# Kernel tuning notes

Hardware: AMD Instinct MI355X
Metric: run time of the kernel (lower is better)

Reference implementation:

```python
import math
import jax, jax.numpy as jnp
import numpy as np

LN_EPS = 1e-5


def _layernorm(x, g, b):
    m = jnp.mean(x, axis=-1, keepdims=True)
    v = jnp.var(x, axis=-1, keepdims=True)
    return (x - m) / jnp.sqrt(v + LN_EPS) * g + b


def setup_inputs() -> dict:
    key = jax.random.key(0)
    ks = jax.random.split(key, 14)
    B, C, H, W = 8, 96, 224, 224
    dim, hidden = 96, int(96 * 4.0)

    def lin(k, i, o):
        return jax.random.normal(k, (i, o), jnp.float32) * 0.02

    return {
        "x": jax.random.normal(ks[0], (B, C, H, W), jnp.float32),
        "entropy_map": jax.random.uniform(ks[1], (B, 1, H, W), jnp.float32),
        "beta": jnp.float32(1.0),
        "wq": lin(ks[2], dim, dim), "bq": jnp.zeros((dim,), jnp.float32),
        "wk": lin(ks[3], dim, dim), "bk": jnp.zeros((dim,), jnp.float32),
        "wv": lin(ks[4], dim, dim), "bv": jnp.zeros((dim,), jnp.float32),
        "wo": lin(ks[5], dim, dim), "bo": jnp.zeros((dim,), jnp.float32),
        "ln1_g": jnp.ones((dim,), jnp.float32), "ln1_b": jnp.zeros((dim,), jnp.float32),
        "ln2_g": jnp.ones((dim,), jnp.float32), "ln2_b": jnp.zeros((dim,), jnp.float32),
        "w_fc1": lin(ks[6], dim, hidden), "b_fc1": jnp.zeros((hidden,), jnp.float32),
        "w_fc2": lin(ks[7], hidden, dim), "b_fc2": jnp.zeros((dim,), jnp.float32),
    }


def reference(x, entropy_map, beta, wq, bq, wk, bk, wv, bv, wo, bo,
              ln1_g, ln1_b, ln2_g, ln2_b, w_fc1, b_fc1, w_fc2, b_fc2):
    B, C, H, W = x.shape
    ws = 7
    num_heads = 4
    hd = C // num_heads
    nHw, nWw = H // ws, W // ws
    N = ws * ws

    # (B,C,H,W) -> (B,H,W,C), norm1
    xt = jnp.transpose(x, (0, 2, 3, 1))
    xn = _layernorm(xt, ln1_g, ln1_b)

    # window partition -> (B*nW, N, C)
    xw = xn.reshape(B, nHw, ws, nWw, ws, C).transpose(0, 1, 3, 2, 4, 5).reshape(-1, N, C)
    ew = entropy_map.transpose(0, 2, 3, 1).reshape(B, nHw, ws, nWw, ws, 1)
    ew = ew.transpose(0, 1, 3, 2, 4, 5).reshape(-1, N, 1)  # (Bw, N, 1)

    Bw = xw.shape[0]
    q = (jnp.einsum('bnc,cd->bnd', xw, wq) + bq).reshape(Bw, N, num_heads, hd).transpose(0, 2, 1, 3)
    k = (jnp.einsum('bnc,cd->bnd', xw, wk) + bk).reshape(Bw, N, num_heads, hd).transpose(0, 2, 1, 3)
    v = (jnp.einsum('bnc,cd->bnd', xw, wv) + bv).reshape(Bw, N, num_heads, hd).transpose(0, 2, 1, 3)

    scores = jnp.einsum('bhqd,bhkd->bhqk', q, k) / math.sqrt(hd)
    attn = jax.nn.softmax(scores, axis=-1)

    # entropy gating: per-query factor (Bw,1,N,1), then renormalize over keys
    gating = jnp.exp(-beta * ew)[:, None, :, :]
    attn = attn * gating
    attn = attn / (jnp.sum(attn, axis=-1, keepdims=True) + 1e-9)

    out = jnp.einsum('bhqk,bhkd->bhqd', attn, v).transpose(0, 2, 1, 3).reshape(Bw, N, C)
    out = jnp.einsum('bnc,cd->bnd', out, wo) + bo

    # window merge -> (B,H,W,C)
    out = out.reshape(B, nHw, nWw, ws, ws, C).transpose(0, 1, 3, 2, 4, 5).reshape(B, H, W, C)

    x_res = xt + out  # (B,H,W,C)

    # MLP branch
    xn2 = _layernorm(x_res, ln2_g, ln2_b)
    h = jax.nn.gelu(jnp.einsum('bhwc,cd->bhwd', xn2, w_fc1) + b_fc1, approximate=False)
    mlp_out = jnp.einsum('bhwd,dc->bhwc', h, w_fc2) + b_fc2

    x_out = x_res + mlp_out
    return jnp.transpose(x_out, (0, 3, 1, 2))  # (B,C,H,W)
```

## Files before the change

### kernel.cpp

```cpp
#include <hip/hip_runtime.h>
#include <hip/hip_bf16.h>
#include <math.h>

typedef __attribute__((ext_vector_type(8))) short short8;
typedef __attribute__((ext_vector_type(4))) float f32x4;
typedef __attribute__((ext_vector_type(4))) unsigned int uint4v;

struct __align__(8) U2 { unsigned int x, y; };

#define DEVI static __device__ __forceinline__

DEVI unsigned pk1(float f){ unsigned u = __float_as_uint(f); return (u + 0x7fffu + ((u>>16)&1u)) >> 16; }
DEVI unsigned pk2(float a, float b){
  __hip_bfloat162 h = __float22bfloat162_rn(float2{a, b});
  union { __hip_bfloat162 h; unsigned u; } c; c.h = h; return c.u;
}
DEVI float bfu(unsigned hs){ return __uint_as_float((hs & 0xffffu) << 16); }

DEVI short8 lds8(const unsigned short* p){
  union { short8 v; U2 u[2]; } f;
  f.u[0] = *(const U2*)p;
  f.u[1] = *(const U2*)(p + 4);
  return f.v;
}
DEVI short8 mk8(unsigned a, unsigned b, unsigned c, unsigned d){
  union { short8 v; unsigned u[4]; } f; f.u[0]=a; f.u[1]=b; f.u[2]=c; f.u[3]=d; return f.v;
}
DEVI short8 zero8(){ return mk8(0,0,0,0); }
DEVI short8 gfrag(const unsigned short* p){ union { short8 v; uint4v u; } f; f.u = *(const uint4v*)p; return f.v; }
DEVI f32x4 MFMA(short8 a, short8 b, f32x4 c){ return __builtin_amdgcn_mfma_f32_16x16x32_bf16(a, b, c, 0, 0, 0); }
DEVI void st2(unsigned short* p, unsigned lo, unsigned hi){ U2 t; t.x=lo; t.y=hi; *(U2*)p = t; }

DEVI float fastrcp(float x){ float r; asm("v_rcp_f32 %0, %1" : "=v"(r) : "v"(x)); return r; }
DEVI float gelu_f(float v){
  float z2 = fmaf(v*v*v, -0.07135481627f, -1.5957691216f*v);
  return v * fastrcp(1.f + __expf(z2));
}

__global__ __launch_bounds__(256) void prep_kernel(
    const float* __restrict__ wq, const float* __restrict__ wk,
    const float* __restrict__ wv, const float* __restrict__ wo,
    const float* __restrict__ w1, const float* __restrict__ w2,
    unsigned short* __restrict__ wfr)
{
  int i = blockIdx.x * 256 + threadIdx.x;
  if (i >= 110592) return;
  int j = i & 7, lane = (i >> 3) & 63, fr = i >> 9;
  int ln = lane & 15, lg = lane >> 4;
  float v;
  if (fr < 18)      { int s = fr;       int mt = s/3,  kb = s%3;  v = wq[(32*kb + 8*lg + j)*96  + 16*mt + ln] * 0.20412414523193150818f; }
  else if (fr < 36) { int s = fr - 18;  int mt = s/3,  kb = s%3;  v = wk[(32*kb + 8*lg + j)*96  + 16*mt + ln]; }
  else if (fr < 54) { int s = fr - 36;  int mt = s/3,  kb = s%3;  v = wv[(32*kb + 8*lg + j)*96  + 16*mt + ln]; }
  else if (fr < 72) { int s = fr - 54;  int mt = s/3,  kb = s%3;  v = wo[(32*kb + 8*lg + j)*96  + 16*mt + ln]; }
  else if (fr < 144){ int s = fr - 72;  int mt = s/3,  kb = s%3;  v = w1[(32*kb + 8*lg + j)*384 + 16*mt + ln]; }
  else              { int s = fr - 144; int mt = s/12, kb = s%12; v = w2[(32*kb + 8*lg + j)*96  + 16*mt + ln]; }
  wfr[i] = (unsigned short)pk1(v);
}

__global__ __launch_bounds__(256, 3) void attn_kernel(
    const float* __restrict__ x, const float* __restrict__ emap,
    const float* __restrict__ beta_p,
    const float* __restrict__ bq, const float* __restrict__ bk,
    const float* __restrict__ bv, const float* __restrict__ bo,
    const float* __restrict__ g1, const float* __restrict__ b1,
    const unsigned short* __restrict__ wfr,
    unsigned short* __restrict__ xres)
{
  __shared__ __align__(16) char smem[52544];
  unsigned short* XN = (unsigned short*)(smem);
  unsigned short* QS = (unsigned short*)(smem + 12800);
  unsigned short* KS = (unsigned short*)(smem + 25600);
  unsigned short* VT = (unsigned short*)(smem + 38400);

  const int tid = threadIdx.x;
  const int lane = tid & 63;
  const int w = tid >> 6, lg = lane >> 4, ln = lane & 15;

  int bid = blockIdx.x;
  int bw  = ((bid & 7) << 10) | (bid >> 3);
  const int b  = bw >> 10;
  const int rr = bw & 1023;
  const int h0w = (rr >> 5) * 7;
  const int w0w = (rr & 31) * 7;

  const int t = 16*w + ln;

  float xv[24];
  float ewv = 0.f;
  {
    if (t < 49){
      size_t pixloc = (size_t)(h0w + t/7)*224 + w0w + t%7;
      const float* xp = x + (size_t)(b*96 + 4*lg)*50176 + pixloc;
#pragma unroll
      for (int mt = 0; mt < 6; ++mt)
#pragma unroll
        for (int r = 0; r < 4; ++r) xv[mt*4+r] = xp[(size_t)(16*mt + r)*50176];
      ewv = emap[(size_t)b*50176 + pixloc];
    } else {
#pragma unroll
      for (int i = 0; i < 24; ++i) xv[i] = 0.f;
    }
    float s = 0.f, s2 = 0.f;
#pragma unroll
    for (int i = 0; i < 24; ++i){ s += xv[i]; s2 += xv[i]*xv[i]; }
    s  += __shfl_xor(s, 16);  s  += __shfl_xor(s, 32);
    s2 += __shfl_xor(s2, 16); s2 += __shfl_xor(s2, 32);
    float m = s * (1.f/96.f);
    float var = s2 * (1.f/96.f) - m*m;
    float rstd = rsqrtf(var + 1e-5f);
    unsigned short* row = XN + t*100;
    if (t < 49){
#pragma unroll
      for (int mt = 0; mt < 6; ++mt){
        int c0 = 16*mt + 4*lg;
        st2(row + c0,
            pk2((xv[4*mt+0]-m)*rstd*g1[c0+0]+b1[c0+0], (xv[4*mt+1]-m)*rstd*g1[c0+1]+b1[c0+1]),
            pk2((xv[4*mt+2]-m)*rstd*g1[c0+2]+b1[c0+2], (xv[4*mt+3]-m)*rstd*g1[c0+3]+b1[c0+3]));
      }
    } else {
#pragma unroll
      for (int mt = 0; mt < 6; ++mt) st2(row + 16*mt + 4*lg, 0u, 0u);
    }
  }
  __syncthreads();

  {
    short8 bx0 = lds8(XN + t*100 + 0  + 8*lg);
    short8 bx1 = lds8(XN + t*100 + 32 + 8*lg);
    short8 bx2 = lds8(XN + t*100 + 64 + 8*lg);
#pragma unroll
    for (int mt = 0; mt < 6; ++mt){
      int d0 = 16*mt + 4*lg;
      f32x4 aq, ak;
#pragma unroll
      for (int r = 0; r < 4; ++r){ aq[r] = bq[d0+r]*0.20412414523193150818f; ak[r] = bk[d0+r]; }
      aq = MFMA(gfrag(wfr +        (mt*3+0)*512 + lane*8), bx0, aq);
      aq = MFMA(gfrag(wfr +        (mt*3+1)*512 + lane*8), bx1, aq);
      aq = MFMA(gfrag(wfr +        (mt*3+2)*512 + lane*8), bx2, aq);
      ak = MFMA(gfrag(wfr + 9216 + (mt*3+0)*512 + lane*8), bx0, ak);
      ak = MFMA(gfrag(wfr + 9216 + (mt*3+1)*512 + lane*8), bx1, ak);
      ak = MFMA(gfrag(wfr + 9216 + (mt*3+2)*512 + lane*8), bx2, ak);
      st2(QS + t*100 + d0, pk2(aq[0],aq[1]), pk2(aq[2],aq[3]));
      st2(KS + t*100 + d0, pk2(ak[0],ak[1]), pk2(ak[2],ak[3]));
    }
#pragma unroll
    for (int f = 0; f < 6; ++f){
      int fl = f*4 + w;
      int mt = fl / 6, nt = fl % 6;
      float bvv = bv[16*nt + ln];
      f32x4 av; av[0]=bvv; av[1]=bvv; av[2]=bvv; av[3]=bvv;
#pragma unroll
      for (int kb = 0; kb < 3; ++kb)
        av = MFMA(lds8(XN + (16*mt+ln)*100 + 32*kb + 8*lg),
                  gfrag(wfr + 18432 + (nt*3+kb)*512 + lane*8), av);
      st2(VT + (16*nt+ln)*68 + 16*mt + 4*lg, pk2(av[0],av[1]), pk2(av[2],av[3]));
    }
  }
  __syncthreads();

  const float beta = beta_p[0];
  const float gq   = __expf(-beta * ewv);
  const float gfac = gq / (gq + 1e-9f);
  const int  psrcA = ((lg & 1) << 5) + ln;
  const int  psrcB = psrcA + 16;
  const bool phi   = (lg >= 2);

  f32x4 mz;  mz[0]=0.f; mz[1]=0.f; mz[2]=0.f; mz[3]=0.f;
  f32x4 m3;
#pragma unroll
  for (int r = 0; r < 4; ++r) m3[r] = (4*lg + r >= 1) ? -50.f : 0.f;

#pragma unroll
  for (int hp = 0; hp < 2; ++hp){
    const int h0 = 2*hp, h1 = 2*hp + 1;

    short8 bqf0 = (lg < 3) ? lds8(QS + t*100 + 24*h0 + 8*lg) : zero8();
    short8 bqf1 = (lg < 3) ? lds8(QS + t*100 + 24*h1 + 8*lg) : zero8();
    f32x4 sv0[4], sv1[4];
#pragma unroll
    for (int mt = 0; mt < 4; ++mt){
      short8 af0 = (lg < 3) ? lds8(KS + (16*mt+ln)*100 + 24*h0 + 8*lg) : zero8();
      short8 af1 = (lg < 3) ? lds8(KS + (16*mt+ln)*100 + 24*h1 + 8*lg) : zero8();
      f32x4 ci = (mt == 3) ? m3 : mz;
      sv0[mt] = MFMA(af0, bqf0, ci);
      sv1[mt] = MFMA(af1, bqf1, ci);
    }

    float vv0[16], vv1[16];
    float ss0 = 0.f, ss1 = 0.f;
#pragma unroll
    for (int i = 0; i < 16; ++i){
      float e0 = __expf(sv0[i>>2][i&3]); vv0[i] = e0; ss0 += e0;
      float e1 = __expf(sv1[i>>2][i&3]); vv1[i] = e1; ss1 += e1;
    }
    ss0 += __shfl_xor(ss0, 16);  ss1 += __shfl_xor(ss1, 16);
    ss0 += __shfl_xor(ss0, 32);  ss1 += __shfl_xor(ss1, 32);
    float inv0 = gfac * fastrcp(ss0);
    float inv1 = gfac * fastrcp(ss1);

    unsigned pu0[4][2], pu1[4][2];
#pragma unroll
    for (int mt = 0; mt < 4; ++mt){
      pu0[mt][0] = pk2(vv0[4*mt+0], vv0[4*mt+1]);
      pu0[mt][1] = pk2(vv0[4*mt+2], vv0[4*mt+3]);
      pu1[mt][0] = pk2(vv1[4*mt+0], vv1[4*mt+1]);
      pu1[mt][1] = pk2(vv1[4*mt+2], vv1[4*mt+3]);
    }

    unsigned a00=__shfl(pu0[0][0],psrcA), a01=__shfl(pu0[0][1],psrcA);
    unsigned e00=__shfl(pu1[0][0],psrcA), e01=__shfl(pu1[0][1],psrcA);
    unsigned a10=__shfl(pu0[1][0],psrcA), a11=__shfl(pu0[1][1],psrcA);
    unsigned e10=__shfl(pu1[1][0],psrcA), e11=__shfl(pu1[1][1],psrcA);
    unsigned b00=__shfl(pu0[0][0],psrcB), b01=__shfl(pu0[0][1],psrcB);
    unsigned f00=__shfl(pu1[0][0],psrcB), f01=__shfl(pu1[0][1],psrcB);
    unsigned b10=__shfl(pu0[1][0],psrcB), b11=__shfl(pu0[1][1],psrcB);
    unsigned f10=__shfl(pu1[1][0],psrcB), f11=__shfl(pu1[1][1],psrcB);
    short8 pf00 = mk8(phi?a10:a00, phi?a11:a01, phi?b10:b00, phi?b11:b01);
    short8 pf10 = mk8(phi?e10:e00, phi?e11:e01, phi?f10:f00, phi?f11:f01);
    unsigned c00=__shfl(pu0[2][0],psrcA), c01=__shfl(pu0[2][1],psrcA);
    unsigned g00=__shfl(pu1[2][0],psrcA), g01=__shfl(pu1[2][1],psrcA);
    unsigned c10=__shfl(pu0[3][0],psrcA), c11=__shfl(pu0[3][1],psrcA);
    unsigned g10=__shfl(pu1[3][0],psrcA), g11=__shfl(pu1[3][1],psrcA);
    unsigned d00=__shfl(pu0[2][0],psrcB), d01=__shfl(pu0[2][1],psrcB);
    unsigned k00=__shfl(pu1[2][0],psrcB), k01=__shfl(pu1[2][1],psrcB);
    unsigned d10=__shfl(pu0[3][0],psrcB), d11=__shfl(pu0[3][1],psrcB);
    unsigned k10=__shfl(pu1[3][0],psrcB), k11=__shfl(pu1[3][1],psrcB);
    short8 pf01 = mk8(phi?c10:c00, phi?c11:c01, phi?d10:d00, phi?d11:d01);
    short8 pf11 = mk8(phi?g10:g00, phi?g11:g01, phi?k10:k00, phi?k11:k01);

#pragma unroll
    for (int mt = 0; mt < 2; ++mt){
      f32x4 pv0; pv0[0]=0.f; pv0[1]=0.f; pv0[2]=0.f; pv0[3]=0.f;
      f32x4 pv1; pv1[0]=0.f; pv1[1]=0.f; pv1[2]=0.f; pv1[3]=0.f;
      pv0 = MFMA(lds8(VT + (24*h0+16*mt+ln)*68 + 0  + 8*lg), pf00, pv0);
      pv1 = MFMA(lds8(VT + (24*h1+16*mt+ln)*68 + 0  + 8*lg), pf10, pv1);
      pv0 = MFMA(lds8(VT + (24*h0+16*mt+ln)*68 + 32 + 8*lg), pf01, pv0);
      pv1 = MFMA(lds8(VT + (24*h1+16*mt+ln)*68 + 32 + 8*lg), pf11, pv1);
      if (!(mt == 1 && lg >= 2)){
        st2(XN + t*100 + 24*h0 + 16*mt + 4*lg,
            pk2(pv0[0]*inv0, pv0[1]*inv0), pk2(pv0[2]*inv0, pv0[3]*inv0));
        st2(XN + t*100 + 24*h1 + 16*mt + 4*lg,
            pk2(pv1[0]*inv1, pv1[1]*inv1), pk2(pv1[2]*inv1, pv1[3]*inv1));
      }
    }
  }

  {
    f32x4 po[6];
#pragma unroll
    for (int mt = 0; mt < 6; ++mt){
      int c0 = 16*mt + 4*lg;
#pragma unroll
      for (int r = 0; r < 4; ++r) po[mt][r] = bo[c0+r];
    }
#pragma unroll
    for (int kb = 0; kb < 3; ++kb){
      short8 bf_ = lds8(XN + t*100 + 32*kb + 8*lg);
#pragma unroll
      for (int mt = 0; mt < 6; ++mt)
        po[mt] = MFMA(gfrag(wfr + 27648 + (mt*3+kb)*512 + lane*8), bf_, po[mt]);
    }
    if (t < 49){
      size_t pixloc = (size_t)(h0w + t/7)*224 + w0w + t%7;
      unsigned short* xo = xres + ((size_t)b*50176 + pixloc)*96;
#pragma unroll
      for (int mt = 0; mt < 6; ++mt){
        int c0 = 16*mt + 4*lg;
        st2(xo + c0,
            pk2(po[mt][0] + xv[4*mt+0], po[mt][1] + xv[4*mt+1]),
            pk2(po[mt][2] + xv[4*mt+2], po[mt][3] + xv[4*mt+3]));
      }
    }
  }
}

__global__ __launch_bounds__(256, 3) void mlp_kernel(
    const unsigned short* __restrict__ xres,
    const float* __restrict__ g2, const float* __restrict__ b2,
    const float* __restrict__ bf1, const float* __restrict__ bf2,
    const unsigned short* __restrict__ wfr,
    float* __restrict__ out)
{
  __shared__ __align__(16) unsigned short XH[4][6400];
  const int tid = threadIdx.x, lane = tid & 63, w = tid >> 6;
  const int lg = lane >> 4, ln = lane & 15;
  unsigned short* XN2 = &XH[w][0];
  unsigned short* HS  = &XH[w][3200];

  const int tile = blockIdx.x*4 + w;
  const size_t p0 = (size_t)tile * 32;
  const int bimg = (int)(p0 / 50176);
  const size_t pixin = p0 - (size_t)bimg*50176;

#pragma unroll
  for (int s = 0; s < 2; ++s){
    const unsigned* xp = (const unsigned*)(xres + (p0 + 16*s + (size_t)ln)*96 + 24*lg);
    float xv[24];
#pragma unroll
    for (int i = 0; i < 12; ++i){
      unsigned u = xp[i];
      xv[2*i] = bfu(u); xv[2*i+1] = bfu(u >> 16);
    }
    float sm = 0.f, s2 = 0.f;
#pragma unroll
    for (int i = 0; i < 24; ++i){ sm += xv[i]; s2 += xv[i]*xv[i]; }
    sm += __shfl_xor(sm, 16);  sm += __shfl_xor(sm, 32);
    s2 += __shfl_xor(s2, 16);  s2 += __shfl_xor(s2, 32);
    float m = sm * (1.f/96.f);
    float var = s2 * (1.f/96.f) - m*m;
    float rstd = rsqrtf(var + 1e-5f);
    unsigned* w32 = (unsigned*)(XN2 + (16*s + ln)*100 + 24*lg);
#pragma unroll
    for (int i = 0; i < 12; ++i){
      int c = 24*lg + 2*i;
      w32[i] = pk2((xv[2*i]   - m)*rstd*g2[c]   + b2[c],
                   (xv[2*i+1] - m)*rstd*g2[c+1] + b2[c+1]);
    }
  }

  f32x4 oaccA[6], oaccB[6];
#pragma unroll
  for (int mt = 0; mt < 6; ++mt){
    int c0 = 16*mt + 4*lg;
#pragma unroll
    for (int r = 0; r < 4; ++r){ oaccA[mt][r] = bf2[c0+r]; oaccB[mt][r] = bf2[c0+r]; }
  }

  short8 bxA0 = lds8(XN2 + ln*100 + 0  + 8*lg);
  short8 bxA1 = lds8(XN2 + ln*100 + 32 + 8*lg);
  short8 bxA2 = lds8(XN2 + ln*100 + 64 + 8*lg);
  short8 bxB0 = lds8(XN2 + (16+ln)*100 + 0  + 8*lg);
  short8 bxB1 = lds8(XN2 + (16+ln)*100 + 32 + 8*lg);
  short8 bxB2 = lds8(XN2 + (16+ln)*100 + 64 + 8*lg);

#pragma unroll
  for (int p = 0; p < 4; ++p){
#pragma unroll
    for (int mt = 0; mt < 6; ++mt){
      int hg = p*96 + 16*mt + 4*lg;
      f32x4 hA, hB;
#pragma unroll
      for (int r = 0; r < 4; ++r){ hA[r] = bf1[hg+r]; hB[r] = bf1[hg+r]; }
      short8 a0 = gfrag(wfr + 36864 + ((p*6+mt)*3+0)*512 + lane*8);
      short8 a1 = gfrag(wfr + 36864 + ((p*6+mt)*3+1)*512 + lane*8);
      short8 a2 = gfrag(wfr + 36864 + ((p*6+mt)*3+2)*512 + lane*8);
      hA = MFMA(a0, bxA0, hA); hB = MFMA(a0, bxB0, hB);
      hA = MFMA(a1, bxA1, hA); hB = MFMA(a1, bxB1, hB);
      hA = MFMA(a2, bxA2, hA); hB = MFMA(a2, bxB2, hB);
      st2(HS + ln*100 + 16*mt + 4*lg,
          pk2(gelu_f(hA[0]), gelu_f(hA[1])), pk2(gelu_f(hA[2]), gelu_f(hA[3])));
      st2(HS + (16+ln)*100 + 16*mt + 4*lg,
          pk2(gelu_f(hB[0]), gelu_f(hB[1])), pk2(gelu_f(hB[2]), gelu_f(hB[3])));
    }
#pragma unroll
    for (int kb = 0; kb < 3; ++kb){
      short8 bhA = lds8(HS + ln*100      + 32*kb + 8*lg);
      short8 bhB = lds8(HS + (16+ln)*100 + 32*kb + 8*lg);
#pragma unroll
      for (int mt = 0; mt < 6; ++mt){
        short8 af = gfrag(wfr + 73728 + (mt*12 + p*3 + kb)*512 + lane*8);
        oaccA[mt] = MFMA(af, bhA, oaccA[mt]);
        oaccB[mt] = MFMA(af, bhB, oaccB[mt]);
      }
    }
  }

  {
    const unsigned short* xrA = xres + (p0 + (size_t)ln)*96;
    const unsigned short* xrB = xrA + 16*96;
    float* obA = out + (size_t)bimg*96*50176 + pixin + ln;
    float* obB = obA + 16;
#pragma unroll
    for (int mt = 0; mt < 6; ++mt){
      int c0 = 16*mt + 4*lg;
      U2 rA = *(const U2*)(xrA + c0);
      U2 rB = *(const U2*)(xrB + c0);
      obA[(size_t)(c0+0)*50176] = oaccA[mt][0] + bfu(rA.x);
      obA[(size_t)(c0+1)*50176] = oaccA[mt][1] + bfu(rA.x >> 16);
      obA[(size_t)(c0+2)*50176] = oaccA[mt][2] + bfu(rA.y);
      obA[(size_t)(c0+3)*50176] = oaccA[mt][3] + bfu(rA.y >> 16);
      obB[(size_t)(c0+0)*50176] = oaccB[mt][0] + bfu(rB.x);
      obB[(size_t)(c0+1)*50176] = oaccB[mt][1] + bfu(rB.x >> 16);
      obB[(size_t)(c0+2)*50176] = oaccB[mt][2] + bfu(rB.y);
      obB[(size_t)(c0+3)*50176] = oaccB[mt][3] + bfu(rB.y >> 16);
    }
  }
}

extern "C" void kernel_launch(void* const* d_in, const int* in_sizes, int n_in,
                              void* d_out, int out_size, void* d_ws, size_t ws_size,
                              hipStream_t stream) {
  const float* x    = (const float*)d_in[0];
  const float* emap = (const float*)d_in[1];
  const float* beta = (const float*)d_in[2];
  const float* wq   = (const float*)d_in[3];
  const float* bq   = (const float*)d_in[4];
  const float* wk   = (const float*)d_in[5];
  const float* bk   = (const float*)d_in[6];
  const float* wv   = (const float*)d_in[7];
  const float* bv   = (const float*)d_in[8];
  const float* wo   = (const float*)d_in[9];
  const float* bo   = (const float*)d_in[10];
  const float* g1   = (const float*)d_in[11];
  const float* b1   = (const float*)d_in[12];
  const float* g2   = (const float*)d_in[13];
  const float* b2   = (const float*)d_in[14];
  const float* w1   = (const float*)d_in[15];
  const float* bf1  = (const float*)d_in[16];
  const float* w2   = (const float*)d_in[17];
  const float* bf2  = (const float*)d_in[18];

  float* out = (float*)d_out;
  unsigned short* wfr  = (unsigned short*)d_ws;
  unsigned short* xres = (unsigned short*)((char*)d_ws + 262144);

  prep_kernel<<<dim3(432), dim3(256), 0, stream>>>(wq, wk, wv, wo, w1, w2, wfr);
  attn_kernel<<<dim3(8192), dim3(256), 0, stream>>>(
      x, emap, beta, bq, bk, bv, bo, g1, b1, wfr, xres);
  mlp_kernel<<<dim3(3136), dim3(256), 0, stream>>>(
      xres, g2, b2, bf1, bf2, wfr, out);
}
```

Baseline: 349.7 us.

## Shrink attention LDS via buffer aliasing and widen MLP tile to 64 pixels

```diff
diff --git a/kernel.cpp b/kernel.cpp
--- a/kernel.cpp
+++ b/kernel.cpp
@@ -57,7 +57,7 @@
   wfr[i] = (unsigned short)pk1(v);
 }
 
-__global__ __launch_bounds__(256, 3) void attn_kernel(
+__global__ __launch_bounds__(256, 4) void attn_kernel(
     const float* __restrict__ x, const float* __restrict__ emap,
     const float* __restrict__ beta_p,
     const float* __restrict__ bq, const float* __restrict__ bk,
@@ -66,11 +66,11 @@
     const unsigned short* __restrict__ wfr,
     unsigned short* __restrict__ xres)
 {
-  __shared__ __align__(16) char smem[52544];
+  __shared__ __align__(16) char smem[39744];
   unsigned short* XN = (unsigned short*)(smem);
-  unsigned short* QS = (unsigned short*)(smem + 12800);
-  unsigned short* KS = (unsigned short*)(smem + 25600);
-  unsigned short* VT = (unsigned short*)(smem + 38400);
+  unsigned short* VT = (unsigned short*)(smem);
+  unsigned short* QS = (unsigned short*)(smem + 14144);
+  unsigned short* KS = (unsigned short*)(smem + 26944);
 
   const int tid = threadIdx.x;
   const int lane = tid & 63;
@@ -122,12 +122,13 @@
       for (int mt = 0; mt < 6; ++mt) st2(row + 16*mt + 4*lg, 0u, 0u);
     }
   }
+
+  short8 bx0 = lds8(XN + t*100 + 0  + 8*lg);
+  short8 bx1 = lds8(XN + t*100 + 32 + 8*lg);
+  short8 bx2 = lds8(XN + t*100 + 64 + 8*lg);
   __syncthreads();
 
   {
-    short8 bx0 = lds8(XN + t*100 + 0  + 8*lg);
-    short8 bx1 = lds8(XN + t*100 + 32 + 8*lg);
-    short8 bx2 = lds8(XN + t*100 + 64 + 8*lg);
 #pragma unroll
     for (int mt = 0; mt < 6; ++mt){
       int d0 = 16*mt + 4*lg;
@@ -144,16 +145,16 @@
       st2(KS + t*100 + d0, pk2(ak[0],ak[1]), pk2(ak[2],ak[3]));
     }
 #pragma unroll
-    for (int f = 0; f < 6; ++f){
-      int fl = f*4 + w;
-      int mt = fl / 6, nt = fl % 6;
-      float bvv = bv[16*nt + ln];
-      f32x4 av; av[0]=bvv; av[1]=bvv; av[2]=bvv; av[3]=bvv;
-#pragma unroll
-      for (int kb = 0; kb < 3; ++kb)
-        av = MFMA(lds8(XN + (16*mt+ln)*100 + 32*kb + 8*lg),
-                  gfrag(wfr + 18432 + (nt*3+kb)*512 + lane*8), av);
-      st2(VT + (16*nt+ln)*68 + 16*mt + 4*lg, pk2(av[0],av[1]), pk2(av[2],av[3]));
+    for (int mt = 0; mt < 6; ++mt){
+      int d0 = 16*mt + 4*lg;
+      f32x4 av;
+#pragma unroll
+      for (int r = 0; r < 4; ++r) av[r] = bv[d0+r];
+      av = MFMA(gfrag(wfr + 18432 + (mt*3+0)*512 + lane*8), bx0, av);
+      av = MFMA(gfrag(wfr + 18432 + (mt*3+1)*512 + lane*8), bx1, av);
+      av = MFMA(gfrag(wfr + 18432 + (mt*3+2)*512 + lane*8), bx2, av);
+#pragma unroll
+      for (int r = 0; r < 4; ++r) VT[(d0+r)*68 + t] = (unsigned short)pk1(av[r]);
     }
   }
   __syncthreads();
@@ -206,7 +207,6 @@
       pu1[mt][0] = pk2(vv1[4*mt+0], vv1[4*mt+1]);
       pu1[mt][1] = pk2(vv1[4*mt+2], vv1[4*mt+3]);
     }
-
     unsigned a00=__shfl(pu0[0][0],psrcA), a01=__shfl(pu0[0][1],psrcA);
     unsigned e00=__shfl(pu1[0][0],psrcA), e01=__shfl(pu1[0][1],psrcA);
     unsigned a10=__shfl(pu0[1][0],psrcA), a11=__shfl(pu0[1][1],psrcA);
@@ -237,9 +237,9 @@
       pv0 = MFMA(lds8(VT + (24*h0+16*mt+ln)*68 + 32 + 8*lg), pf01, pv0);
       pv1 = MFMA(lds8(VT + (24*h1+16*mt+ln)*68 + 32 + 8*lg), pf11, pv1);
       if (!(mt == 1 && lg >= 2)){
-        st2(XN + t*100 + 24*h0 + 16*mt + 4*lg,
+        st2(QS + t*100 + 24*h0 + 16*mt + 4*lg,
             pk2(pv0[0]*inv0, pv0[1]*inv0), pk2(pv0[2]*inv0, pv0[3]*inv0));
-        st2(XN + t*100 + 24*h1 + 16*mt + 4*lg,
+        st2(QS + t*100 + 24*h1 + 16*mt + 4*lg,
             pk2(pv1[0]*inv1, pv1[1]*inv1), pk2(pv1[2]*inv1, pv1[3]*inv1));
       }
     }
@@ -255,7 +255,7 @@
     }
 #pragma unroll
     for (int kb = 0; kb < 3; ++kb){
-      short8 bf_ = lds8(XN + t*100 + 32*kb + 8*lg);
+      short8 bf_ = lds8(QS + t*100 + 32*kb + 8*lg);
 #pragma unroll
       for (int mt = 0; mt < 6; ++mt)
         po[mt] = MFMA(gfrag(wfr + 27648 + (mt*3+kb)*512 + lane*8), bf_, po[mt]);
@@ -274,115 +274,116 @@
   }
 }
 
-__global__ __launch_bounds__(256, 3) void mlp_kernel(
+__global__ __launch_bounds__(256, 2) void mlp_kernel(
     const unsigned short* __restrict__ xres,
     const float* __restrict__ g2, const float* __restrict__ b2,
     const float* __restrict__ bf1, const float* __restrict__ bf2,
     const unsigned short* __restrict__ wfr,
     float* __restrict__ out)
 {
-  __shared__ __align__(16) unsigned short XH[4][6400];
+  __shared__ __align__(16) unsigned short HSall[4][6400];
   const int tid = threadIdx.x, lane = tid & 63, w = tid >> 6;
   const int lg = lane >> 4, ln = lane & 15;
-  unsigned short* XN2 = &XH[w][0];
-  unsigned short* HS  = &XH[w][3200];
+  unsigned short* HS = &HSall[w][0];
 
   const int tile = blockIdx.x*4 + w;
-  const size_t p0 = (size_t)tile * 32;
+  const size_t p0 = (size_t)tile * 64;
   const int bimg = (int)(p0 / 50176);
   const size_t pixin = p0 - (size_t)bimg*50176;
 
-#pragma unroll
-  for (int s = 0; s < 2; ++s){
-    const unsigned* xp = (const unsigned*)(xres + (p0 + 16*s + (size_t)ln)*96 + 24*lg);
+  short8 bx[4][3];
+#pragma unroll
+  for (int s = 0; s < 4; ++s){
+    const unsigned short* xp = xres + (p0 + 16*s + (size_t)ln)*96 + 8*lg;
+    uint4v raw0 = *(const uint4v*)(xp);
+    uint4v raw1 = *(const uint4v*)(xp + 32);
+    uint4v raw2 = *(const uint4v*)(xp + 64);
     float xv[24];
 #pragma unroll
-    for (int i = 0; i < 12; ++i){
-      unsigned u = xp[i];
-      xv[2*i] = bfu(u); xv[2*i+1] = bfu(u >> 16);
+    for (int q = 0; q < 4; ++q){
+      xv[0 + 2*q] = bfu(raw0[q]);  xv[1 + 2*q]  = bfu(raw0[q] >> 16);
+      xv[8 + 2*q] = bfu(raw1[q]);  xv[9 + 2*q]  = bfu(raw1[q] >> 16);
+      xv[16 + 2*q]= bfu(raw2[q]);  xv[17 + 2*q] = bfu(raw2[q] >> 16);
     }
     float sm = 0.f, s2 = 0.f;
 #pragma unroll
     for (int i = 0; i < 24; ++i){ sm += xv[i]; s2 += xv[i]*xv[i]; }
     sm += __shfl_xor(sm, 16);  sm += __shfl_xor(sm, 32);
     s2 += __shfl_xor(s2, 16);  s2 += __shfl_xor(s2, 32);
-    float m = sm * (1.f/96.f);
-    float var = s2 * (1.f/96.f) - m*m;
+    float mean = sm * (1.f/96.f);
+    float var  = s2 * (1.f/96.f) - mean*mean;
     float rstd = rsqrtf(var + 1e-5f);
-    unsigned* w32 = (unsigned*)(XN2 + (16*s + ln)*100 + 24*lg);
-#pragma unroll
-    for (int i = 0; i < 12; ++i){
-      int c = 24*lg + 2*i;
-      w32[i] = pk2((xv[2*i]   - m)*rstd*g2[c]   + b2[c],
-                   (xv[2*i+1] - m)*rstd*g2[c+1] + b2[c+1]);
-    }
-  }
-
-  f32x4 oaccA[6], oaccB[6];
-#pragma unroll
-  for (int mt = 0; mt < 6; ++mt){
-    int c0 = 16*mt + 4*lg;
-#pragma unroll
-    for (int r = 0; r < 4; ++r){ oaccA[mt][r] = bf2[c0+r]; oaccB[mt][r] = bf2[c0+r]; }
-  }
-
-  short8 bxA0 = lds8(XN2 + ln*100 + 0  + 8*lg);
-  short8 bxA1 = lds8(XN2 + ln*100 + 32 + 8*lg);
-  short8 bxA2 = lds8(XN2 + ln*100 + 64 + 8*lg);
-  short8 bxB0 = lds8(XN2 + (16+ln)*100 + 0  + 8*lg);
-  short8 bxB1 = lds8(XN2 + (16+ln)*100 + 32 + 8*lg);
-  short8 bxB2 = lds8(XN2 + (16+ln)*100 + 64 + 8*lg);
+#pragma unroll
+    for (int m = 0; m < 3; ++m){
+      const float* gp = g2 + 32*m + 8*lg;
+      const float* bp = b2 + 32*m + 8*lg;
+      unsigned u0 = pk2((xv[m*8+0]-mean)*rstd*gp[0]+bp[0], (xv[m*8+1]-mean)*rstd*gp[1]+bp[1]);
+      unsigned u1 = pk2((xv[m*8+2]-mean)*rstd*gp[2]+bp[2], (xv[m*8+3]-mean)*rstd*gp[3]+bp[3]);
+      unsigned u2 = pk2((xv[m*8+4]-mean)*rstd*gp[4]+bp[4], (xv[m*8+5]-mean)*rstd*gp[5]+bp[5]);
+      unsigned u3 = pk2((xv[m*8+6]-mean)*rstd*gp[6]+bp[6], (xv[m*8+7]-mean)*rstd*gp[7]+bp[7]);
+      bx[s][m] = mk8(u0, u1, u2, u3);
+    }
+  }
+
+  f32x4 oacc[4][6];
+#pragma unroll
+  for (int s = 0; s < 4; ++s)
+#pragma unroll
+    for (int mt = 0; mt < 6; ++mt){
+      int c0 = 16*mt + 4*lg;
+#pragma unroll
+      for (int r = 0; r < 4; ++r) oacc[s][mt][r] = bf2[c0+r];
+    }
 
 #pragma unroll
   for (int p = 0; p < 4; ++p){
 #pragma unroll
     for (int mt = 0; mt < 6; ++mt){
       int hg = p*96 + 16*mt + 4*lg;
-      f32x4 hA, hB;
-#pragma unroll
-      for (int r = 0; r < 4; ++r){ hA[r] = bf1[hg+r]; hB[r] = bf1[hg+r]; }
       short8 a0 = gfrag(wfr + 36864 + ((p*6+mt)*3+0)*512 + lane*8);
       short8 a1 = gfrag(wfr + 36864 + ((p*6+mt)*3+1)*512 + lane*8);
       short8 a2 = gfrag(wfr + 36864 + ((p*6+mt)*3+2)*512 + lane*8);
-      hA = MFMA(a0, bxA0, hA); hB = MFMA(a0, bxB0, hB);
-      hA = MFMA(a1, bxA1, hA); hB = MFMA(a1, bxB1, hB);
-      hA = MFMA(a2, bxA2, hA); hB = MFMA(a2, bxB2, hB);
-      st2(HS + ln*100 + 16*mt + 4*lg,
-          pk2(gelu_f(hA[0]), gelu_f(hA[1])), pk2(gelu_f(hA[2]), gelu_f(hA[3])));
-      st2(HS + (16+ln)*100 + 16*mt + 4*lg,
-          pk2(gelu_f(hB[0]), gelu_f(hB[1])), pk2(gelu_f(hB[2]), gelu_f(hB[3])));
+#pragma unroll
+      for (int s = 0; s < 4; ++s){
+        f32x4 h;
+#pragma unroll
+        for (int r = 0; r < 4; ++r) h[r] = bf1[hg+r];
+        h = MFMA(a0, bx[s][0], h);
+        h = MFMA(a1, bx[s][1], h);
+        h = MFMA(a2, bx[s][2], h);
+        st2(HS + (16*s+ln)*100 + 16*mt + 4*lg,
+            pk2(gelu_f(h[0]), gelu_f(h[1])), pk2(gelu_f(h[2]), gelu_f(h[3])));
+      }
     }
 #pragma unroll
     for (int kb = 0; kb < 3; ++kb){
-      short8 bhA = lds8(HS + ln*100      + 32*kb + 8*lg);
-      short8 bhB = lds8(HS + (16+ln)*100 + 32*kb + 8*lg);
+      short8 bh0 = lds8(HS + (     ln)*100 + 32*kb + 8*lg);
+      short8 bh1 = lds8(HS + (16 + ln)*100 + 32*kb + 8*lg);
+      short8 bh2 = lds8(HS + (32 + ln)*100 + 32*kb + 8*lg);
+      short8 bh3 = lds8(HS + (48 + ln)*100 + 32*kb + 8*lg);
 #pragma unroll
       for (int mt = 0; mt < 6; ++mt){
         short8 af = gfrag(wfr + 73728 + (mt*12 + p*3 + kb)*512 + lane*8);
-        oaccA[mt] = MFMA(af, bhA, oaccA[mt]);
-        oaccB[mt] = MFMA(af, bhB, oaccB[mt]);
+        oacc[0][mt] = MFMA(af, bh0, oacc[0][mt]);
+        oacc[1][mt] = MFMA(af, bh1, oacc[1][mt]);
+        oacc[2][mt] = MFMA(af, bh2, oacc[2][mt]);
+        oacc[3][mt] = MFMA(af, bh3, oacc[3][mt]);
       }
     }
   }
 
-  {
-    const unsigned short* xrA = xres + (p0 + (size_t)ln)*96;
-    const unsigned short* xrB = xrA + 16*96;
-    float* obA = out + (size_t)bimg*96*50176 + pixin + ln;
-    float* obB = obA + 16;
+#pragma unroll
+  for (int s = 0; s < 4; ++s){
+    const unsigned short* xr = xres + (p0 + 16*s + (size_t)ln)*96;
+    float* ob = out + (size_t)bimg*96*50176 + pixin + 16*s + ln;
 #pragma unroll
     for (int mt = 0; mt < 6; ++mt){
       int c0 = 16*mt + 4*lg;
-      U2 rA = *(const U2*)(xrA + c0);
-      U2 rB = *(const U2*)(xrB + c0);
-      obA[(size_t)(c0+0)*50176] = oaccA[mt][0] + bfu(rA.x);
-      obA[(size_t)(c0+1)*50176] = oaccA[mt][1] + bfu(rA.x >> 16);
-      obA[(size_t)(c0+2)*50176] = oaccA[mt][2] + bfu(rA.y);
-      obA[(size_t)(c0+3)*50176] = oaccA[mt][3] + bfu(rA.y >> 16);
-      obB[(size_t)(c0+0)*50176] = oaccB[mt][0] + bfu(rB.x);
-      obB[(size_t)(c0+1)*50176] = oaccB[mt][1] + bfu(rB.x >> 16);
-      obB[(size_t)(c0+2)*50176] = oaccB[mt][2] + bfu(rB.y);
-      obB[(size_t)(c0+3)*50176] = oaccB[mt][3] + bfu(rB.y >> 16);
+      U2 rv = *(const U2*)(xr + c0);
+      ob[(size_t)(c0+0)*50176] = oacc[s][mt][0] + bfu(rv.x);
+      ob[(size_t)(c0+1)*50176] = oacc[s][mt][1] + bfu(rv.x >> 16);
+      ob[(size_t)(c0+2)*50176] = oacc[s][mt][2] + bfu(rv.y);
+      ob[(size_t)(c0+3)*50176] = oacc[s][mt][3] + bfu(rv.y >> 16);
     }
   }
 }
@@ -417,6 +418,6 @@
   prep_kernel<<<dim3(432), dim3(256), 0, stream>>>(wq, wk, wv, wo, w1, w2, wfr);
   attn_kernel<<<dim3(8192), dim3(256), 0, stream>>>(
       x, emap, beta, bq, bk, bv, bo, g1, b1, wfr, xres);
-  mlp_kernel<<<dim3(3136), dim3(256), 0, stream>>>(
+  mlp_kernel<<<dim3(1568), dim3(256), 0, stream>>>(
       xres, g2, b2, bf1, bf2, wfr, out);
 }
```

Result: slower. 477.7 us (+36.6%).

## Reuse LN fragments for V, overlay VT on XN, and stage P through LDS

Applied to the files above, without the earlier changes.

```diff
diff --git a/kernel.cpp b/kernel.cpp
--- a/kernel.cpp
+++ b/kernel.cpp
@@ -66,11 +66,12 @@
     const unsigned short* __restrict__ wfr,
     unsigned short* __restrict__ xres)
 {
-  __shared__ __align__(16) char smem[52544];
+  __shared__ __align__(16) char smem[48448];
   unsigned short* XN = (unsigned short*)(smem);
-  unsigned short* QS = (unsigned short*)(smem + 12800);
-  unsigned short* KS = (unsigned short*)(smem + 25600);
-  unsigned short* VT = (unsigned short*)(smem + 38400);
+  unsigned short* VT = (unsigned short*)(smem);
+  unsigned short* QS = (unsigned short*)(smem + 14144);
+  unsigned short* KS = (unsigned short*)(smem + 26944);
+  unsigned short* PB = (unsigned short*)(smem + 39744);
 
   const int tid = threadIdx.x;
   const int lane = tid & 63;
@@ -122,12 +123,13 @@
       for (int mt = 0; mt < 6; ++mt) st2(row + 16*mt + 4*lg, 0u, 0u);
     }
   }
+
+  short8 bx0 = lds8(XN + t*100 + 0  + 8*lg);
+  short8 bx1 = lds8(XN + t*100 + 32 + 8*lg);
+  short8 bx2 = lds8(XN + t*100 + 64 + 8*lg);
   __syncthreads();
 
   {
-    short8 bx0 = lds8(XN + t*100 + 0  + 8*lg);
-    short8 bx1 = lds8(XN + t*100 + 32 + 8*lg);
-    short8 bx2 = lds8(XN + t*100 + 64 + 8*lg);
 #pragma unroll
     for (int mt = 0; mt < 6; ++mt){
       int d0 = 16*mt + 4*lg;
@@ -144,16 +146,16 @@
       st2(KS + t*100 + d0, pk2(ak[0],ak[1]), pk2(ak[2],ak[3]));
     }
 #pragma unroll
-    for (int f = 0; f < 6; ++f){
-      int fl = f*4 + w;
-      int mt = fl / 6, nt = fl % 6;
-      float bvv = bv[16*nt + ln];
-      f32x4 av; av[0]=bvv; av[1]=bvv; av[2]=bvv; av[3]=bvv;
-#pragma unroll
-      for (int kb = 0; kb < 3; ++kb)
-        av = MFMA(lds8(XN + (16*mt+ln)*100 + 32*kb + 8*lg),
-                  gfrag(wfr + 18432 + (nt*3+kb)*512 + lane*8), av);
-      st2(VT + (16*nt+ln)*68 + 16*mt + 4*lg, pk2(av[0],av[1]), pk2(av[2],av[3]));
+    for (int mt = 0; mt < 6; ++mt){
+      int d0 = 16*mt + 4*lg;
+      f32x4 av;
+#pragma unroll
+      for (int r = 0; r < 4; ++r) av[r] = bv[d0+r];
+      av = MFMA(gfrag(wfr + 18432 + (mt*3+0)*512 + lane*8), bx0, av);
+      av = MFMA(gfrag(wfr + 18432 + (mt*3+1)*512 + lane*8), bx1, av);
+      av = MFMA(gfrag(wfr + 18432 + (mt*3+2)*512 + lane*8), bx2, av);
+#pragma unroll
+      for (int r = 0; r < 4; ++r) VT[(d0+r)*68 + t] = (unsigned short)pk1(av[r]);
     }
   }
   __syncthreads();
@@ -161,14 +163,13 @@
   const float beta = beta_p[0];
   const float gq   = __expf(-beta * ewv);
   const float gfac = gq / (gq + 1e-9f);
-  const int  psrcA = ((lg & 1) << 5) + ln;
-  const int  psrcB = psrcA + 16;
-  const bool phi   = (lg >= 2);
 
   f32x4 mz;  mz[0]=0.f; mz[1]=0.f; mz[2]=0.f; mz[3]=0.f;
   f32x4 m3;
 #pragma unroll
   for (int r = 0; r < 4; ++r) m3[r] = (4*lg + r >= 1) ? -50.f : 0.f;
+
+  unsigned short* PBw = PB + (w*16 + ln)*68;
 
 #pragma unroll
   for (int hp = 0; hp < 2; ++hp){
@@ -198,35 +199,19 @@
     float inv0 = gfac * fastrcp(ss0);
     float inv1 = gfac * fastrcp(ss1);
 
-    unsigned pu0[4][2], pu1[4][2];
-#pragma unroll
-    for (int mt = 0; mt < 4; ++mt){
-      pu0[mt][0] = pk2(vv0[4*mt+0], vv0[4*mt+1]);
-      pu0[mt][1] = pk2(vv0[4*mt+2], vv0[4*mt+3]);
-      pu1[mt][0] = pk2(vv1[4*mt+0], vv1[4*mt+1]);
-      pu1[mt][1] = pk2(vv1[4*mt+2], vv1[4*mt+3]);
-    }
-
-    unsigned a00=__shfl(pu0[0][0],psrcA), a01=__shfl(pu0[0][1],psrcA);
-    unsigned e00=__shfl(pu1[0][0],psrcA), e01=__shfl(pu1[0][1],psrcA);
-    unsigned a10=__shfl(pu0[1][0],psrcA), a11=__shfl(pu0[1][1],psrcA);
-    unsigned e10=__shfl(pu1[1][0],psrcA), e11=__shfl(pu1[1][1],psrcA);
-    unsigned b00=__shfl(pu0[0][0],psrcB), b01=__shfl(pu0[0][1],psrcB);
-    unsigned f00=__shfl(pu1[0][0],psrcB), f01=__shfl(pu1[0][1],psrcB);
-    unsigned b10=__shfl(pu0[1][0],psrcB), b11=__shfl(pu0[1][1],psrcB);
-    unsigned f10=__shfl(pu1[1][0],psrcB), f11=__shfl(pu1[1][1],psrcB);
-    short8 pf00 = mk8(phi?a10:a00, phi?a11:a01, phi?b10:b00, phi?b11:b01);
-    short8 pf10 = mk8(phi?e10:e00, phi?e11:e01, phi?f10:f00, phi?f11:f01);
-    unsigned c00=__shfl(pu0[2][0],psrcA), c01=__shfl(pu0[2][1],psrcA);
-    unsigned g00=__shfl(pu1[2][0],psrcA), g01=__shfl(pu1[2][1],psrcA);
-    unsigned c10=__shfl(pu0[3][0],psrcA), c11=__shfl(pu0[3][1],psrcA);
-    unsigned g10=__shfl(pu1[3][0],psrcA), g11=__shfl(pu1[3][1],psrcA);
-    unsigned d00=__shfl(pu0[2][0],psrcB), d01=__shfl(pu0[2][1],psrcB);
-    unsigned k00=__shfl(pu1[2][0],psrcB), k01=__shfl(pu1[2][1],psrcB);
-    unsigned d10=__shfl(pu0[3][0],psrcB), d11=__shfl(pu0[3][1],psrcB);
-    unsigned k10=__shfl(pu1[3][0],psrcB), k11=__shfl(pu1[3][1],psrcB);
-    short8 pf01 = mk8(phi?c10:c00, phi?c11:c01, phi?d10:d00, phi?d11:d01);
-    short8 pf11 = mk8(phi?g10:g00, phi?g11:g01, phi?k10:k00, phi?k11:k01);
+#pragma unroll
+    for (int mt = 0; mt < 4; ++mt)
+      st2(PBw + 16*mt + 4*lg,
+          pk2(vv0[4*mt+0], vv0[4*mt+1]), pk2(vv0[4*mt+2], vv0[4*mt+3]));
+    short8 pf00 = lds8(PBw + 0  + 8*lg);
+    short8 pf01 = lds8(PBw + 32 + 8*lg);
+
+#pragma unroll
+    for (int mt = 0; mt < 4; ++mt)
+      st2(PBw + 16*mt + 4*lg,
+          pk2(vv1[4*mt+0], vv1[4*mt+1]), pk2(vv1[4*mt+2], vv1[4*mt+3]));
+    short8 pf10 = lds8(PBw + 0  + 8*lg);
+    short8 pf11 = lds8(PBw + 32 + 8*lg);
 
 #pragma unroll
     for (int mt = 0; mt < 2; ++mt){
@@ -237,9 +222,9 @@
       pv0 = MFMA(lds8(VT + (24*h0+16*mt+ln)*68 + 32 + 8*lg), pf01, pv0);
       pv1 = MFMA(lds8(VT + (24*h1+16*mt+ln)*68 + 32 + 8*lg), pf11, pv1);
       if (!(mt == 1 && lg >= 2)){
-        st2(XN + t*100 + 24*h0 + 16*mt + 4*lg,
+        st2(QS + t*100 + 24*h0 + 16*mt + 4*lg,
             pk2(pv0[0]*inv0, pv0[1]*inv0), pk2(pv0[2]*inv0, pv0[3]*inv0));
-        st2(XN + t*100 + 24*h1 + 16*mt + 4*lg,
+        st2(QS + t*100 + 24*h1 + 16*mt + 4*lg,
             pk2(pv1[0]*inv1, pv1[1]*inv1), pk2(pv1[2]*inv1, pv1[3]*inv1));
       }
     }
@@ -255,7 +240,7 @@
     }
 #pragma unroll
     for (int kb = 0; kb < 3; ++kb){
-      short8 bf_ = lds8(XN + t*100 + 32*kb + 8*lg);
+      short8 bf_ = lds8(QS + t*100 + 32*kb + 8*lg);
 #pragma unroll
       for (int mt = 0; mt < 6; ++mt)
         po[mt] = MFMA(gfrag(wfr + 27648 + (mt*3+kb)*512 + lane*8), bf_, po[mt]);
```

Result: no change. 353.7 us (+1.2%).
